# Optimization experiments

Measured on AMD Instinct MI355X. Metric: run time of the kernel, lower is better.

The kernel has to match this reference:

```python
import jax, jax.numpy as jnp
import numpy as np

V = 25   # NTU joints
NE = 5   # number of hyper-edge types


def setup_inputs() -> dict:
    key = jax.random.key(0)
    ks = jax.random.split(key, 8)
    N, C, T = 64, 12, 300
    x = jax.random.normal(ks[0], (N, C, T, V), dtype=jnp.float32)
    # binary incidence matrices [V, E] with E == V, as in the NTU hyper-edge tables
    hs = [jax.random.bernoulli(ks[1 + i], 0.2, (V, V)).astype(jnp.float32) for i in range(NE)]
    in_ch, out_ch = 3, 64
    w_mlp = jax.random.normal(ks[6], (out_ch, in_ch * NE), dtype=jnp.float32) * (1.0 / np.sqrt(in_ch * NE))
    b_mlp = jnp.zeros((out_ch,), dtype=jnp.float32)
    return {"x": x, "h_local": hs[0], "h_center": hs[1], "h_figl": hs[2],
            "h_figr": hs[3], "h_hand": hs[4], "w_mlp": w_mlp, "b_mlp": b_mlp}


def _normalized_aggregate(w, h):
    # w: [N, T, E], h: [V, E] (E == V)
    degree_v = jnp.einsum('ve,bte->btv', h, w)
    # pow(d, -0.5): inf at d==0 and nan at d<0 are both zeroed in the original
    dv_pos = degree_v > 0
    degree_v = jnp.where(dv_pos, jax.lax.rsqrt(jnp.where(dv_pos, degree_v, 1.0)), 0.0)
    degree_e = jnp.sum(h, axis=0)                      # [E]
    de_nz = degree_e != 0
    degree_e = jnp.where(de_nz, 1.0 / jnp.where(de_nz, degree_e, 1.0), 0.0)
    # fused dh * w * degree_e chain: [N, T, V, E]
    dhwb = degree_v[..., None] * h[None, None] * w[:, :, None, :] * degree_e
    dhwbht = jnp.einsum('btve,ue->btvu', dhwb, h)      # [N, T, V, V]
    return dhwbht * degree_v[:, :, None, :]


def reference(x, h_local, h_center, h_figl, h_figr, h_hand, w_mlp, b_mlp):
    ws = (x[:, 6], x[:, 7], x[:, 9], x[:, 10], x[:, 11])
    hs = (h_local, h_center, h_figl, h_figr, h_hand)
    hwh_cat = jnp.concatenate([_normalized_aggregate(w, h) for w, h in zip(ws, hs)], axis=-2)  # [N,T,5V,V]
    feat = x[:, :3]                                    # [N, 3, T, V]
    N, C, T, Vv = feat.shape
    support = jnp.einsum('btvu,bctu->bctv', hwh_cat, feat)          # [N, C, T, 5V]
    support = support.reshape(N, C, T, NE, Vv).transpose(0, 3, 1, 2, 4).reshape(N, NE * C, T, Vv)
    out = jnp.einsum('oi,bitv->botv', w_mlp, support) + b_mlp[None, :, None, None]
    return jax.nn.relu(out)
```

## Files before the change

### kernel.cpp

```cpp
#include <hip/hip_runtime.h>

#define NE  5
#define V   25
#define NT  300
#define NC  12
#define CO  64
#define WPB 4
#define GX  38

typedef float f4 __attribute__((ext_vector_type(4)));
typedef float f2 __attribute__((ext_vector_type(2)));

#define WSYNC() do { asm volatile("s_waitcnt lgkmcnt(0)" ::: "memory"); \
                     __builtin_amdgcn_sched_barrier(0); } while (0)

__device__ __forceinline__ float hsel(unsigned m, int e, float w) {
    int s = ((int)(m << (31 - e))) >> 31;
    return __int_as_float(__float_as_int(w) & s);
}

#define OW   0
#define ODV  224
#define OG   364
#define OB   504
#define OFP  924
#define OST  1344
#define SCRF 2364

#define STROW(r) (OST + (r)*20 + (((r) >> 3) & 7)*4)

__global__ __launch_bounds__(256, 4) void hyper_main(
    const float* __restrict__ x,
    const float* __restrict__ h0, const float* __restrict__ h1,
    const float* __restrict__ h2, const float* __restrict__ h3,
    const float* __restrict__ h4,
    const float* __restrict__ wmlp, const float* __restrict__ bmlp,
    float* __restrict__ out)
{
    __shared__ unsigned RM[125];
    __shared__ unsigned CM[125];
    __shared__ float    DE[125];
    __shared__ __align__(16) float SCR[WPB][SCRF];

    const int tid  = threadIdx.x;
    const int lane = tid & 63;
    const int wid  = tid >> 6;
    const int b    = blockIdx.y;

    if (tid < 125) {
        int i = tid / 25, v = tid % 25;
        const float* hp = (i==0)?h0:(i==1)?h1:(i==2)?h2:(i==3)?h3:h4;
        unsigned m = 0;
        for (int e = 0; e < V; ++e) if (hp[v*V + e] != 0.f) m |= (1u << e);
        RM[tid] = m;
    } else if (tid < 250) {
        int idx = tid - 125, i = idx / 25, e = idx % 25;
        const float* hp = (i==0)?h0:(i==1)?h1:(i==2)?h2:(i==3)?h3:h4;
        unsigned m = 0; float s = 0.f;
        for (int u = 0; u < V; ++u) {
            float hv = hp[u*V + e];
            s += hv;
            if (hv != 0.f) m |= (1u << u);
        }
        CM[idx] = m;
        DE[idx] = (s != 0.f) ? __fdiv_rn(1.f, s) : 0.f;
    }
    __syncthreads();

    const int pp = blockIdx.x * WPB + wid;
    const bool wvalid = (pp < NT/2);

    float* S = SCR[wid];

    const float* xb[4]; int lo[4];
    {
        #pragma unroll
        for (int r = 0; r < 4; ++r) {
            int q  = r*64 + lane;
            int qq = (q < 200) ? q : 0;
            int ch = qq / 25, e = qq % 25;
            int xc = (ch < 5) ? (ch + 6 + (ch >= 2 ? 1 : 0)) : (ch - 5);
            lo[r] = OW + ch*28 + e;
            xb[r] = x + (size_t)(b*NC + xc)*NT*V + e;
        }
    }
    const bool act3 = (lane < 8);

    float pf0, pf1, pf2, pf3;
    {
        int t0 = wvalid ? 2 * pp : 0;
        pf0 = xb[0][t0*V]; pf1 = xb[1][t0*V];
        pf2 = xb[2][t0*V]; pf3 = xb[3][t0*V];
    }

    for (int tp = 0; tp < 2; ++tp) {

        S[lo[0]] = pf0; S[lo[1]] = pf1; S[lo[2]] = pf2;
        if (act3) S[lo[3]] = pf3;
        WSYNC();

        if (tp == 0) {
            int tn = wvalid ? (2*pp + 1) : 0;
            pf0 = xb[0][tn*V]; pf1 = xb[1][tn*V];
            pf2 = xb[2][tn*V]; pf3 = xb[3][tn*V];
        }

        for (int r = 0; r < 2; ++r) {
            int idx = r*64 + lane;
            if (idx < 125) {
                int i = idx / 25, v = idx % 25;
                unsigned m = RM[idx];
                const float* wi = S + OW + i*28;
                f4 w0 = *(const f4*)(wi+0),  w1 = *(const f4*)(wi+4),
                   w2 = *(const f4*)(wi+8),  w3 = *(const f4*)(wi+12),
                   w4 = *(const f4*)(wi+16), w5 = *(const f4*)(wi+20),
                   w6 = *(const f4*)(wi+24);
                float L0 = 0.f, L1 = 0.f, L2 = 0.f, L3 = 0.f;
                L0=__fadd_rn(L0,hsel(m, 0,w0.x)); L1=__fadd_rn(L1,hsel(m, 1,w0.y));
                L2=__fadd_rn(L2,hsel(m, 2,w0.z)); L3=__fadd_rn(L3,hsel(m, 3,w0.w));
                L0=__fadd_rn(L0,hsel(m, 4,w1.x)); L1=__fadd_rn(L1,hsel(m, 5,w1.y));
                L2=__fadd_rn(L2,hsel(m, 6,w1.z)); L3=__fadd_rn(L3,hsel(m, 7,w1.w));
                L0=__fadd_rn(L0,hsel(m, 8,w2.x)); L1=__fadd_rn(L1,hsel(m, 9,w2.y));
                L2=__fadd_rn(L2,hsel(m,10,w2.z)); L3=__fadd_rn(L3,hsel(m,11,w2.w));
                L0=__fadd_rn(L0,hsel(m,12,w3.x)); L1=__fadd_rn(L1,hsel(m,13,w3.y));
                L2=__fadd_rn(L2,hsel(m,14,w3.z)); L3=__fadd_rn(L3,hsel(m,15,w3.w));
                L0=__fadd_rn(L0,hsel(m,16,w4.x)); L1=__fadd_rn(L1,hsel(m,17,w4.y));
                L2=__fadd_rn(L2,hsel(m,18,w4.z)); L3=__fadd_rn(L3,hsel(m,19,w4.w));
                L0=__fadd_rn(L0,hsel(m,20,w5.x)); L1=__fadd_rn(L1,hsel(m,21,w5.y));
                L2=__fadd_rn(L2,hsel(m,22,w5.z)); L3=__fadd_rn(L3,hsel(m,23,w5.w));
                float s = __fadd_rn(__fadd_rn(L0,L1), __fadd_rn(L2,L3));
                s = __fadd_rn(s, hsel(m, 24, w6.x));
                float dvv = (s > 0.f) ? (float)(1.0 / sqrt((double)s)) : 0.f;
                S[ODV + i*28 + v] = dvv;
                S[OG  + i*28 + v] = S[OW + i*28 + v] * DE[idx];
                float f0 = S[OW + 5*28 + v];
                float f1 = S[OW + 6*28 + v];
                float f2v = S[OW + 7*28 + v];
                S[OB + (0*5+i)*28 + v] = dvv * f0;
                S[OB + (1*5+i)*28 + v] = dvv * f1;
                S[OB + (2*5+i)*28 + v] = dvv * f2v;
            }
        }
        WSYNC();

        for (int r = 0; r < 2; ++r) {
            int idx = r*64 + lane;
            if (idx < 125) {
                int i = idx / 25, e = idx % 25;
                unsigned m = CM[idx];
                const float* bp = S + OB + i*28;
                float a0 = 0.f, a1 = 0.f, a2 = 0.f;
                while (m) {
                    int u[5]; bool vl[5];
                    #pragma unroll
                    for (int j = 0; j < 5; ++j) {
                        vl[j] = (m != 0u);
                        u[j]  = __builtin_ctz(m | 0x02000000u);
                        m &= m - 1;
                    }
                    float b0[5], b1[5], b2[5];
                    #pragma unroll
                    for (int j = 0; j < 5; ++j) {
                        b0[j] = bp[u[j]];
                        b1[j] = bp[140 + u[j]];
                        b2[j] = bp[280 + u[j]];
                    }
                    #pragma unroll
                    for (int j = 0; j < 5; ++j) {
                        a0 += vl[j] ? b0[j] : 0.f;
                        a1 += vl[j] ? b1[j] : 0.f;
                        a2 += vl[j] ? b2[j] : 0.f;
                    }
                }
                float gg = S[OG + i*28 + e];
                S[OFP + (i*3+0)*28 + e] = a0 * gg;
                S[OFP + (i*3+1)*28 + e] = a1 * gg;
                S[OFP + (i*3+2)*28 + e] = a2 * gg;
            }
        }
        WSYNC();

        for (int r = 0; r < 2; ++r) {
            int idx = r*64 + lane;
            if (idx < 125) {
                int i = idx / 25, v = idx % 25;
                unsigned m = RM[idx];
                const float* fp = S + OFP + i*3*28;
                float a0 = 0.f, a1 = 0.f, a2 = 0.f;
                while (m) {
                    int u[5]; bool vl[5];
                    #pragma unroll
                    for (int j = 0; j < 5; ++j) {
                        vl[j] = (m != 0u);
                        u[j]  = __builtin_ctz(m | 0x02000000u);
                        m &= m - 1;
                    }
                    float b0[5], b1[5], b2[5];
                    #pragma unroll
                    for (int j = 0; j < 5; ++j) {
                        b0[j] = fp[u[j]];
                        b1[j] = fp[28 + u[j]];
                        b2[j] = fp[56 + u[j]];
                    }
                    #pragma unroll
                    for (int j = 0; j < 5; ++j) {
                        a0 += vl[j] ? b0[j] : 0.f;
                        a1 += vl[j] ? b1[j] : 0.f;
                        a2 += vl[j] ? b2[j] : 0.f;
                    }
                }
                float dd = S[ODV + i*28 + v];
                float* st = S + STROW(tp*25 + v) + i*3;
                st[0] = a0 * dd; st[1] = a1 * dd; st[2] = a2 * dd;
            }
        }
        WSYNC();
    }

    __syncthreads();

    if (lane < 50) {
        const int o0 = wid * 16;
        #pragma unroll
        for (int g = 0; g < 2; ++g) {
            int q  = 2*g + (lane >= 25 ? 1 : 0);
            int rr = (lane >= 25) ? 2*(lane - 25) : 2*lane;
            const float* SQ = SCR[q];
            const float* ra = SQ + STROW(rr);
            const float* rb = SQ + STROW(rr + 1);
            f4 a0 = *(const f4*)(ra+0), a1 = *(const f4*)(ra+4),
               a2 = *(const f4*)(ra+8), a3 = *(const f4*)(ra+12);
            f4 b0 = *(const f4*)(rb+0), b1 = *(const f4*)(rb+4),
               b2 = *(const f4*)(rb+8), b3 = *(const f4*)(rb+12);
            f2 k0 = {a0.x, b0.x}, k1 = {a0.y, b0.y}, k2 = {a0.z, b0.z},
               k3 = {a0.w, b0.w}, k4 = {a1.x, b1.x}, k5 = {a1.y, b1.y},
               k6 = {a1.z, b1.z}, k7 = {a1.w, b1.w}, k8 = {a2.x, b2.x},
               k9 = {a2.y, b2.y}, k10 = {a2.z, b2.z}, k11 = {a2.w, b2.w},
               k12 = {a3.x, b3.x}, k13 = {a3.y, b3.y}, k14 = {a3.z, b3.z};
            int pg = blockIdx.x*200 + q*50 + rr;
            bool ok = (pg < 7500);
            float* ob = out + (size_t)b*CO*7500 + pg;
            #pragma unroll 4
            for (int oi = 0; oi < 16; ++oi) {
                int o = o0 + oi;
                const float* wm = wmlp + o*15;
                float bb = bmlp[o];
                f2 acc = {bb, bb};
                acc += k0  * wm[ 0]; acc += k1  * wm[ 1];
                acc += k2  * wm[ 2]; acc += k3  * wm[ 3];
                acc += k4  * wm[ 4]; acc += k5  * wm[ 5];
                acc += k6  * wm[ 6]; acc += k7  * wm[ 7];
                acc += k8  * wm[ 8]; acc += k9  * wm[ 9];
                acc += k10 * wm[10]; acc += k11 * wm[11];
                acc += k12 * wm[12]; acc += k13 * wm[13];
                acc += k14 * wm[14];
                f2 res = {fmaxf(acc.x, 0.f), fmaxf(acc.y, 0.f)};
                if (ok) *(f2*)(ob + (size_t)o*7500) = res;
            }
        }
    }
}

extern "C" void kernel_launch(void* const* d_in, const int* in_sizes, int n_in,
                              void* d_out, int out_size, void* d_ws, size_t ws_size,
                              hipStream_t stream) {
    const float* x    = (const float*)d_in[0];
    const float* h0   = (const float*)d_in[1];
    const float* h1   = (const float*)d_in[2];
    const float* h2   = (const float*)d_in[3];
    const float* h3   = (const float*)d_in[4];
    const float* h4   = (const float*)d_in[5];
    const float* wmlp = (const float*)d_in[6];
    const float* bmlp = (const float*)d_in[7];
    float* out = (float*)d_out;

    hyper_main<<<dim3(GX, 64, 1), dim3(256,1,1), 0, stream>>>(
        x, h0, h1, h2, h3, h4, wmlp, bmlp, out);
}
```

Before: 78.57 us.

## Store support in channel-interleaved timestep-pair layout and use nontemporal output stores

Changes the shared-memory staging of per-joint support values from row-per-(t,v) with padding to a per-joint layout that interleaves the two timesteps per channel. The epilogue can then read each lane's data with eight aligned 16-byte loads that feed the packed two-wide FMAs directly, with no repacking. Output writes become scalar nontemporal stores, one per timestep, so a lane's pair of outputs is no longer a single contiguous 8-byte store. The extra padding slots are zeroed by otherwise idle lanes in a third loop iteration.

```diff
diff --git a/kernel.cpp b/kernel.cpp
--- a/kernel.cpp
+++ b/kernel.cpp
@@ -24,10 +24,8 @@
 #define OG   364
 #define OB   504
 #define OFP  924
-#define OST  1344
-#define SCRF 2364
-
-#define STROW(r) (OST + (r)*20 + (((r) >> 3) & 7)*4)
+#define OSTP 1344
+#define SCRF 2244
 
 __global__ __launch_bounds__(256, 4) void hyper_main(
     const float* __restrict__ x,
@@ -180,7 +178,7 @@
         }
         WSYNC();
 
-        for (int r = 0; r < 2; ++r) {
+        for (int r = 0; r < 3; ++r) {
             int idx = r*64 + lane;
             if (idx < 125) {
                 int i = idx / 25, v = idx % 25;
@@ -210,8 +208,12 @@
                     }
                 }
                 float dd = S[ODV + i*28 + v];
-                float* st = S + STROW(tp*25 + v) + i*3;
-                st[0] = a0 * dd; st[1] = a1 * dd; st[2] = a2 * dd;
+                float* stp = S + OSTP + v*36 + tp;
+                stp[(3*i+0)*2] = a0 * dd;
+                stp[(3*i+1)*2] = a1 * dd;
+                stp[(3*i+2)*2] = a2 * dd;
+            } else if (idx < 150) {
+                S[OSTP + (idx - 125)*36 + 30 + tp] = 0.f;
             }
         }
         WSYNC();
@@ -221,41 +223,44 @@
 
     if (lane < 50) {
         const int o0 = wid * 16;
+        const int j  = (lane >= 25) ? (lane - 25) : lane;
         #pragma unroll
         for (int g = 0; g < 2; ++g) {
-            int q  = 2*g + (lane >= 25 ? 1 : 0);
-            int rr = (lane >= 25) ? 2*(lane - 25) : 2*lane;
-            const float* SQ = SCR[q];
-            const float* ra = SQ + STROW(rr);
-            const float* rb = SQ + STROW(rr + 1);
-            f4 a0 = *(const f4*)(ra+0), a1 = *(const f4*)(ra+4),
-               a2 = *(const f4*)(ra+8), a3 = *(const f4*)(ra+12);
-            f4 b0 = *(const f4*)(rb+0), b1 = *(const f4*)(rb+4),
-               b2 = *(const f4*)(rb+8), b3 = *(const f4*)(rb+12);
-            f2 k0 = {a0.x, b0.x}, k1 = {a0.y, b0.y}, k2 = {a0.z, b0.z},
-               k3 = {a0.w, b0.w}, k4 = {a1.x, b1.x}, k5 = {a1.y, b1.y},
-               k6 = {a1.z, b1.z}, k7 = {a1.w, b1.w}, k8 = {a2.x, b2.x},
-               k9 = {a2.y, b2.y}, k10 = {a2.z, b2.z}, k11 = {a2.w, b2.w},
-               k12 = {a3.x, b3.x}, k13 = {a3.y, b3.y}, k14 = {a3.z, b3.z};
-            int pg = blockIdx.x*200 + q*50 + rr;
-            bool ok = (pg < 7500);
-            float* ob = out + (size_t)b*CO*7500 + pg;
+            int q = 2*g + (lane >= 25 ? 1 : 0);
+            bool ok = (blockIdx.x*WPB + q) < NT/2;
+            const float* base = SCR[q] + OSTP + j*36;
+            f4 c0 = *(const f4*)(base+ 0), c1 = *(const f4*)(base+ 4),
+               c2 = *(const f4*)(base+ 8), c3 = *(const f4*)(base+12),
+               c4 = *(const f4*)(base+16), c5 = *(const f4*)(base+20),
+               c6 = *(const f4*)(base+24), c7 = *(const f4*)(base+28);
+            float* ob = out + (size_t)b*CO*7500 + (size_t)blockIdx.x*200 + q*50 + j;
             #pragma unroll 4
             for (int oi = 0; oi < 16; ++oi) {
                 int o = o0 + oi;
                 const float* wm = wmlp + o*15;
                 float bb = bmlp[o];
                 f2 acc = {bb, bb};
-                acc += k0  * wm[ 0]; acc += k1  * wm[ 1];
-                acc += k2  * wm[ 2]; acc += k3  * wm[ 3];
-                acc += k4  * wm[ 4]; acc += k5  * wm[ 5];
-                acc += k6  * wm[ 6]; acc += k7  * wm[ 7];
-                acc += k8  * wm[ 8]; acc += k9  * wm[ 9];
-                acc += k10 * wm[10]; acc += k11 * wm[11];
-                acc += k12 * wm[12]; acc += k13 * wm[13];
-                acc += k14 * wm[14];
-                f2 res = {fmaxf(acc.x, 0.f), fmaxf(acc.y, 0.f)};
-                if (ok) *(f2*)(ob + (size_t)o*7500) = res;
+                acc += (f2){c0.x, c0.y} * wm[ 0];
+                acc += (f2){c0.z, c0.w} * wm[ 1];
+                acc += (f2){c1.x, c1.y} * wm[ 2];
+                acc += (f2){c1.z, c1.w} * wm[ 3];
+                acc += (f2){c2.x, c2.y} * wm[ 4];
+                acc += (f2){c2.z, c2.w} * wm[ 5];
+                acc += (f2){c3.x, c3.y} * wm[ 6];
+                acc += (f2){c3.z, c3.w} * wm[ 7];
+                acc += (f2){c4.x, c4.y} * wm[ 8];
+                acc += (f2){c4.z, c4.w} * wm[ 9];
+                acc += (f2){c5.x, c5.y} * wm[10];
+                acc += (f2){c5.z, c5.w} * wm[11];
+                acc += (f2){c6.x, c6.y} * wm[12];
+                acc += (f2){c6.z, c6.w} * wm[13];
+                acc += (f2){c7.x, c7.y} * wm[14];
+                if (ok) {
+                    __builtin_nontemporal_store(fmaxf(acc.x, 0.f),
+                                                ob + (size_t)o*7500);
+                    __builtin_nontemporal_store(fmaxf(acc.y, 0.f),
+                                                ob + (size_t)o*7500 + 25);
+                }
             }
         }
     }
```

Measured after the change: 78.22 us. No clear change (-0.5%).
